# Performance work log

Hardware: AMD Instinct MI355X
Metric: run time of the kernel (lower is better)

## Reference

```python
import jax, jax.numpy as jnp
import numpy as np

DIM = 512
NUM_HEADS = 16
HEAD_DIM = DIM // NUM_HEADS  # 32
SCALE = HEAD_DIM ** -0.5
B_, N = 1024, 49  # num_windows*batch, window_size**2


def setup_inputs() -> dict:
    key = jax.random.key(0)
    ks = jax.random.split(key, 12)
    s = DIM ** -0.5
    return {
        "x": jax.random.normal(ks[0], (B_, N, DIM), jnp.float32),
        "x2": jax.random.normal(ks[1], (B_, N, DIM), jnp.float32),
        "x3": jax.random.normal(ks[2], (B_, N, DIM), jnp.float32),
        # Linear weights stored as [in, out] (y = x @ W + b), same math as torch Linear
        "Wqkv": jax.random.normal(ks[3], (DIM, 3 * DIM), jnp.float32) * s,
        "bqkv": jnp.zeros((3 * DIM,), jnp.float32),
        "Wqkv2": jax.random.normal(ks[4], (DIM, 3 * DIM), jnp.float32) * s,
        "bqkv2": jnp.zeros((3 * DIM,), jnp.float32),
        "Wgw": jax.random.normal(ks[5], (DIM, DIM), jnp.float32) * s,
        "bgw": jnp.zeros((DIM,), jnp.float32),
        "Wproj": jax.random.normal(ks[6], (DIM, DIM), jnp.float32) * s,
        "bproj": jnp.zeros((DIM,), jnp.float32),
        "a": jnp.zeros((1,), jnp.float32),
    }


def reference(x, x2, x3, Wqkv, bqkv, Wqkv2, bqkv2, Wgw, bgw, Wproj, bproj, a):
    B, Nn, C = x.shape
    H, D = NUM_HEADS, HEAD_DIM
    # qkv from x: only k is actually used downstream
    qkv = (x @ Wqkv + bqkv).reshape(B, Nn, 3, H, D)
    k = jnp.transpose(qkv[:, :, 1], (0, 2, 1, 3))  # [B,H,N,D]
    # qkv2 from x3: q1 (gated query) and v1 (value + residual)
    qkv1 = (x3 @ Wqkv2 + bqkv2).reshape(B, Nn, 3, H, D)
    q1 = jnp.transpose(qkv1[:, :, 0], (0, 2, 1, 3))  # [B,H,N,D]
    v1 = jnp.transpose(qkv1[:, :, 2], (0, 2, 1, 3))  # [B,H,N,D]
    # gate from x2
    gw = jnp.transpose((x2 @ Wgw + bgw).reshape(B, Nn, H, D), (0, 2, 1, 3))
    q = q1 * SCALE * gw
    attn = jax.nn.softmax(jnp.einsum("bhnd,bhmd->bhnm", q, k), axis=-1)
    out = jnp.einsum("bhnm,bhmd->bhnd", attn, v1) + v1 * a
    out = jnp.transpose(out, (0, 2, 1, 3)).reshape(B, Nn, C)
    return out @ Wproj + bproj
```

## Files before the change

### kernel.cpp

```cpp
#include <hip/hip_runtime.h>

#define MR 50176
#define DIMC 512
#define NWIN 49
#define NBATCH 1024
#define NHEADS 16
#define ATTN_SCALE 0.17677669529663689f

typedef short bf16x8 __attribute__((ext_vector_type(8)));
typedef float f32x4 __attribute__((ext_vector_type(4)));
typedef unsigned int u32;

__device__ __forceinline__ unsigned short f2bf(float f) {
  union { float f; u32 u; } v; v.f = f;
  u32 u = v.u;
  u += 0x7FFFu + ((u >> 16) & 1u);
  return (unsigned short)(u >> 16);
}
__device__ __forceinline__ float bits_f(u32 u) {
  union { u32 u; float f; } v; v.u = u; return v.f;
}

__device__ __forceinline__ size_t pk_chunk(int r, int c) {
  return (((size_t)(r >> 3) * 8 + (c >> 3)) * 64 +
          ((r & 7) * 8 + ((c & 7) ^ (r & 7)))) << 4;
}

typedef const __attribute__((address_space(1))) u32* gp_t;
typedef __attribute__((address_space(3))) u32* lp_t;
__device__ __forceinline__ void glds16(const void* g, void* l) {
  __builtin_amdgcn_global_load_lds((gp_t)g, (lp_t)l, 16, 0, 0);
}

__global__ __launch_bounds__(256) void prep_w_pack(
    const float* __restrict__ Wqkv, const float* __restrict__ Wqkv2,
    const float* __restrict__ Wgw, const float* __restrict__ Wproj,
    short* __restrict__ Wp) {
  const int tid = blockIdx.x * 256 + threadIdx.x;
  const int li = tid & 63, gl = tid >> 6;
  const int kline = gl & 7, group = gl >> 3;
  const int rr = li >> 3, pp = li & 7;
  const int row = group * 8 + rr;
  const int k = kline * 64 + ((pp ^ rr) << 3);
  const int n = row & 511, mat = row >> 9;
  const float* W; int ldw, col;
  if (mat == 0)      { W = Wqkv;  ldw = 1536; col = 512 + n; }
  else if (mat == 1) { W = Wqkv2; ldw = 1536; col = n; }
  else if (mat == 2) { W = Wqkv2; ldw = 1536; col = 1024 + n; }
  else if (mat == 3) { W = Wgw;   ldw = 512;  col = n; }
  else               { W = Wproj; ldw = 512;  col = n; }
  unsigned short h[8];
#pragma unroll
  for (int j = 0; j < 8; ++j) h[j] = f2bf(W[(size_t)(k + j) * ldw + col]);
  u32 w0 = (u32)h[0] | ((u32)h[1] << 16);
  u32 w1 = (u32)h[2] | ((u32)h[3] << 16);
  u32 w2 = (u32)h[4] | ((u32)h[5] << 16);
  u32 w3 = (u32)h[6] | ((u32)h[7] << 16);
  ((uint4*)Wp)[tid] = make_uint4(w0, w1, w2, w3);
}

struct GemmCfg {
  const short* A[4];
  const float* Af[4];
  const float* bias[4];
  short* out[4];
  int wrow0[4];
};

template <int LNX, bool OUT_F32, bool CONVA>
__global__ __launch_bounds__(256) void gemm_glds(
    GemmCfg cfg, const short* __restrict__ Wp, float* __restrict__ outf) {
  __shared__ short As[128 * 64];
  __shared__ short Bs[128 * 64];

  const int t = threadIdx.x, w = t >> 6, lane = t & 63;
  const int l15 = lane & 15, q = lane >> 4;
  const int wm = w >> 1, wn = w & 1;
  const int id = blockIdx.x;
  const int xcd = id & 7, slot = id >> 3;
  const int bx = slot & ((1 << LNX) - 1);
  const int y = xcd + ((slot >> LNX) << 3);
  const int row0 = y * 128;
  const int unit = bx >> 2, sub = bx & 3;
  const float* bias = cfg.bias[unit];
  short* outb = cfg.out[unit];
  const int nw0 = cfg.wrow0[unit] + sub * 128;
  const int col0 = sub * 128;

  f32x4 acc[4][4];
#pragma unroll
  for (int i = 0; i < 4; ++i)
#pragma unroll
    for (int j = 0; j < 4; ++j) acc[i][j] = {0.f, 0.f, 0.f, 0.f};

  const size_t lb = (size_t)lane * 16;
  const int r7 = l15 & 7, hi8 = l15 >> 3;

  if constexpr (CONVA) {
    const int rr = lane >> 3, pp = lane & 7;
    const float* abase =
        cfg.Af[unit] + (size_t)(row0 + w * 32 + rr) * DIMC + ((pp ^ rr) << 3);
    float4 ar[4][2];
#pragma unroll
    for (int jj = 0; jj < 4; ++jj) {
      const float* s = abase + (size_t)jj * 8 * DIMC;
      ar[jj][0] = *(const float4*)s;
      ar[jj][1] = *(const float4*)(s + 4);
    }
    for (int kt = 0; kt < 8; ++kt) {
      asm volatile("s_barrier" ::: "memory");
#pragma unroll
      for (int jj = 0; jj < 4; ++jj) {
        const int rg = w * 4 + jj;
        const char* gb =
            (const char*)Wp + ((((size_t)(nw0 >> 3) + rg) * 8 + kt) << 10);
        glds16(gb + lb, &Bs[(size_t)rg << 9]);
      }
      asm volatile("s_waitcnt vmcnt(4)" ::: "memory");
#pragma unroll
      for (int jj = 0; jj < 4; ++jj) {
        u32 w0 = (u32)f2bf(ar[jj][0].x) | ((u32)f2bf(ar[jj][0].y) << 16);
        u32 w1 = (u32)f2bf(ar[jj][0].z) | ((u32)f2bf(ar[jj][0].w) << 16);
        u32 w2 = (u32)f2bf(ar[jj][1].x) | ((u32)f2bf(ar[jj][1].y) << 16);
        u32 w3 = (u32)f2bf(ar[jj][1].z) | ((u32)f2bf(ar[jj][1].w) << 16);
        *(uint4*)&As[(((size_t)(w * 4 + jj)) << 9) + (size_t)lane * 8] =
            make_uint4(w0, w1, w2, w3);
      }
      if (kt < 7) {
#pragma unroll
        for (int jj = 0; jj < 4; ++jj) {
          const float* s = abase + (size_t)jj * 8 * DIMC + (kt + 1) * 64;
          ar[jj][0] = *(const float4*)s;
          ar[jj][1] = *(const float4*)(s + 4);
        }
        asm volatile("s_waitcnt vmcnt(8) lgkmcnt(0)" ::: "memory");
      } else {
        asm volatile("s_waitcnt vmcnt(0) lgkmcnt(0)" ::: "memory");
      }
      asm volatile("s_barrier" ::: "memory");
#pragma unroll
      for (int s = 0; s < 2; ++s) {
        const int sw = ((s * 4 + q) ^ r7);
        const int pos = (r7 * 8 + sw) * 8;
        bf16x8 af[4], bfr[4];
#pragma unroll
        for (int i = 0; i < 4; ++i)
          af[i] = *(const bf16x8*)&As[((wm * 8 + i * 2 + hi8) << 9) + pos];
#pragma unroll
        for (int j = 0; j < 4; ++j)
          bfr[j] = *(const bf16x8*)&Bs[((wn * 8 + j * 2 + hi8) << 9) + pos];
#pragma unroll
        for (int i = 0; i < 4; ++i)
#pragma unroll
          for (int j = 0; j < 4; ++j)
            acc[i][j] = __builtin_amdgcn_mfma_f32_16x16x32_bf16(
                af[i], bfr[j], acc[i][j], 0, 0, 0);
      }
    }
  } else {
    const short* Ap = cfg.A[unit];
    for (int kt = 0; kt < 8; ++kt) {
      __syncthreads();
#pragma unroll
      for (int jj = 0; jj < 4; ++jj) {
        const int rg = w * 4 + jj;
        const char* ga =
            (const char*)Ap + ((((size_t)(row0 >> 3) + rg) * 8 + kt) << 10);
        glds16(ga + lb, &As[(size_t)rg << 9]);
        const char* gb =
            (const char*)Wp + ((((size_t)(nw0 >> 3) + rg) * 8 + kt) << 10);
        glds16(gb + lb, &Bs[(size_t)rg << 9]);
      }
      __syncthreads();
#pragma unroll
      for (int s = 0; s < 2; ++s) {
        const int sw = ((s * 4 + q) ^ r7);
        const int pos = (r7 * 8 + sw) * 8;
        bf16x8 af[4], bfr[4];
#pragma unroll
        for (int i = 0; i < 4; ++i)
          af[i] = *(const bf16x8*)&As[((wm * 8 + i * 2 + hi8) << 9) + pos];
#pragma unroll
        for (int j = 0; j < 4; ++j)
          bfr[j] = *(const bf16x8*)&Bs[((wn * 8 + j * 2 + hi8) << 9) + pos];
#pragma unroll
        for (int i = 0; i < 4; ++i)
#pragma unroll
          for (int j = 0; j < 4; ++j)
            acc[i][j] = __builtin_amdgcn_mfma_f32_16x16x32_bf16(
                af[i], bfr[j], acc[i][j], 0, 0, 0);
      }
    }
  }

#pragma unroll
  for (int j = 0; j < 4; ++j) {
    const int C = col0 + wn * 64 + j * 16 + l15;
    const float bv = bias[C];
#pragma unroll
    for (int i = 0; i < 4; ++i) {
#pragma unroll
      for (int r = 0; r < 4; ++r) {
        const int R = row0 + wm * 64 + i * 16 + q * 4 + r;
        const float val = acc[i][j][r] + bv;
        if constexpr (OUT_F32)
          outf[(size_t)R * DIMC + C] = val;
        else
          *(short*)((char*)outb + pk_chunk(R, C >> 3) + ((C & 7) << 1)) =
              (short)f2bf(val);
      }
    }
  }
}

__global__ __launch_bounds__(256) void attn_mfma(
    const short* __restrict__ kbuf, const short* __restrict__ qbuf,
    const short* __restrict__ vbuf, const short* __restrict__ gbuf,
    const float* __restrict__ a_scalar, short* __restrict__ obuf) {
  __shared__ short pls[4][64 * 40];
  __shared__ short vls[4][32 * 72];

  const int t = threadIdx.x;
  const int w = t >> 6, lane = t & 63;
  const int l15 = lane & 15, q = lane >> 4;
  const int wid = blockIdx.x * 4 + w;
  const int b = wid >> 4, h = wid & 15;
  const int row0 = b * NWIN;
  const float aval = a_scalar[0];
  short* P = pls[w];
  short* VT = vls[w];

#pragma unroll
  for (int it = 0; it < 5; ++it) {
    int off = (it * 64 + lane) * 8;
    if (off < 32 * 72) *(uint4*)&VT[off] = make_uint4(0u, 0u, 0u, 0u);
  }

  bf16x8 kf[4];
#pragma unroll
  for (int mj = 0; mj < 4; ++mj) {
    int m = mj * 16 + l15; if (m > 48) m = 48;
    kf[mj] = *(const bf16x8*)((const char*)kbuf + pk_chunk(row0 + m, h * 4 + q));
  }
  bf16x8 qf[4];
#pragma unroll
  for (int mi = 0; mi < 4; ++mi) {
    int n = mi * 16 + l15; if (n > 48) n = 48;
    const size_t off = pk_chunk(row0 + n, h * 4 + q);
    uint4 qa = *(const uint4*)((const char*)qbuf + off);
    uint4 ga = *(const uint4*)((const char*)gbuf + off);
    u32* qa_ = (u32*)&qa;
    u32* ga_ = (u32*)&ga;
    uint4 res; u32* r_ = (u32*)&res;
#pragma unroll
    for (int jj = 0; jj < 4; ++jj) {
      float lo = bits_f(qa_[jj] << 16) * bits_f(ga_[jj] << 16);
      float hi = bits_f(qa_[jj] & 0xffff0000u) * bits_f(ga_[jj] & 0xffff0000u);
      r_[jj] = (u32)f2bf(lo) | ((u32)f2bf(hi) << 16);
    }
    qf[mi] = *(bf16x8*)&res;
  }
#pragma unroll
  for (int it = 0; it < 4; ++it) {
    int chunk = it * 64 + lane;
    if (chunk < 196) {
      int n = chunk >> 2, dcq = chunk & 3;
      uint4 v = *(const uint4*)((const char*)vbuf + pk_chunk(row0 + n, h * 4 + dcq));
      const short* vs = (const short*)&v;
#pragma unroll
      for (int j = 0; j < 8; ++j) VT[(dcq * 8 + j) * 72 + n] = vs[j];
    }
  }

  f32x4 s[4][4];
#pragma unroll
  for (int mi = 0; mi < 4; ++mi)
#pragma unroll
    for (int nj = 0; nj < 4; ++nj) {
      f32x4 z = {0.f, 0.f, 0.f, 0.f};
      s[mi][nj] = __builtin_amdgcn_mfma_f32_16x16x32_bf16(qf[mi], kf[nj], z, 0, 0, 0);
    }

#pragma unroll
  for (int mi = 0; mi < 4; ++mi)
#pragma unroll
    for (int nj = 0; nj < 4; ++nj) {
      const bool valid = (nj * 16 + l15) < NWIN;
#pragma unroll
      for (int r = 0; r < 4; ++r)
        s[mi][nj][r] = valid ? __expf(ATTN_SCALE * s[mi][nj][r]) : 0.f;
    }

  float lsum[4][4];
#pragma unroll
  for (int mi = 0; mi < 4; ++mi)
#pragma unroll
    for (int r = 0; r < 4; ++r) {
      float part = s[mi][0][r] + s[mi][1][r] + s[mi][2][r] + s[mi][3][r];
      part += __shfl_xor(part, 1, 64);
      part += __shfl_xor(part, 2, 64);
      part += __shfl_xor(part, 4, 64);
      part += __shfl_xor(part, 8, 64);
      lsum[mi][r] = part;
    }

  f32x4 o[4][2];
#pragma unroll
  for (int mi = 0; mi < 4; ++mi)
#pragma unroll
    for (int dj = 0; dj < 2; ++dj) o[mi][dj] = {0.f, 0.f, 0.f, 0.f};

#pragma unroll
  for (int c = 0; c < 2; ++c) {
#pragma unroll
    for (int mi = 0; mi < 4; ++mi)
#pragma unroll
      for (int njh = 0; njh < 2; ++njh) {
        const int nj = c * 2 + njh;
        const int m = nj * 16 + l15;
#pragma unroll
        for (int r = 0; r < 4; ++r) {
          const int n = mi * 16 + q * 4 + r;
          float val = s[mi][nj][r];
          if (m == n) val += aval * lsum[mi][r];
          P[n * 40 + njh * 16 + l15] = (short)f2bf(val);
        }
      }
    bf16x8 bfr[2];
#pragma unroll
    for (int dj = 0; dj < 2; ++dj)
      bfr[dj] = *(const bf16x8*)&VT[(dj * 16 + l15) * 72 + c * 32 + q * 8];
#pragma unroll
    for (int mi = 0; mi < 4; ++mi) {
      bf16x8 af = *(const bf16x8*)&P[(mi * 16 + l15) * 40 + q * 8];
#pragma unroll
      for (int dj = 0; dj < 2; ++dj)
        o[mi][dj] = __builtin_amdgcn_mfma_f32_16x16x32_bf16(af, bfr[dj],
                                                            o[mi][dj], 0, 0, 0);
    }
  }

#pragma unroll
  for (int mi = 0; mi < 4; ++mi)
#pragma unroll
    for (int r = 0; r < 4; ++r) {
      const int n = mi * 16 + q * 4 + r;
      if (n < NWIN) {
        const float rl = 1.0f / lsum[mi][r];
#pragma unroll
        for (int dj = 0; dj < 2; ++dj) {
          const int d = dj * 16 + l15;
          *(short*)((char*)obuf + pk_chunk(row0 + n, h * 4 + (d >> 3)) +
                    ((d & 7) << 1)) = (short)f2bf(o[mi][dj][r] * rl);
        }
      }
    }
}

extern "C" void kernel_launch(void* const* d_in, const int* in_sizes, int n_in,
                              void* d_out, int out_size, void* d_ws,
                              size_t ws_size, hipStream_t stream) {
  const float* x     = (const float*)d_in[0];
  const float* x2    = (const float*)d_in[1];
  const float* x3    = (const float*)d_in[2];
  const float* Wqkv  = (const float*)d_in[3];
  const float* bqkv  = (const float*)d_in[4];
  const float* Wqkv2 = (const float*)d_in[5];
  const float* bqkv2 = (const float*)d_in[6];
  const float* Wgw   = (const float*)d_in[7];
  const float* bgw   = (const float*)d_in[8];
  const float* Wproj = (const float*)d_in[9];
  const float* bproj = (const float*)d_in[10];
  const float* a     = (const float*)d_in[11];

  char* ws = (char*)d_ws;
  const size_t WTSZ = (size_t)2560 * DIMC * sizeof(short);
  const size_t BSZ  = (size_t)MR * DIMC * sizeof(short);
  short* wt_all = (short*)ws;

  short* kbuf = (short*)(ws + WTSZ);
  short* qbuf = (short*)(ws + WTSZ + BSZ);
  short* vbuf = (short*)(ws + WTSZ + 2 * BSZ);
  short* gbuf = (short*)(ws + WTSZ + 3 * BSZ);
  short* obuf = (short*)(ws + WTSZ + 4 * BSZ);

  prep_w_pack<<<640, 256, 0, stream>>>(Wqkv, Wqkv2, Wgw, Wproj, wt_all);

  GemmCfg s1 = {};
  s1.Af[0] = x;  s1.Af[1] = x3; s1.Af[2] = x3; s1.Af[3] = x2;
  s1.bias[0] = bqkv + 512; s1.bias[1] = bqkv2;
  s1.bias[2] = bqkv2 + 1024; s1.bias[3] = bgw;
  s1.out[0] = kbuf; s1.out[1] = qbuf; s1.out[2] = vbuf; s1.out[3] = gbuf;
  s1.wrow0[0] = 0; s1.wrow0[1] = 512; s1.wrow0[2] = 1024; s1.wrow0[3] = 1536;
  gemm_glds<4, false, true><<<16 * 392, 256, 0, stream>>>(s1, wt_all, nullptr);

  attn_mfma<<<(NBATCH * NHEADS) / 4, 256, 0, stream>>>(kbuf, qbuf, vbuf,
                                                       gbuf, a, obuf);

  GemmCfg pj = {};
  pj.A[0] = obuf; pj.bias[0] = bproj; pj.out[0] = nullptr; pj.wrow0[0] = 2048;
  gemm_glds<2, true, false><<<4 * 392, 256, 0, stream>>>(pj, wt_all,
                                                         (float*)d_out);
}
```

Measured before the change: 612.7 us.

## Double-buffer LDS tiles in GEMM to overlap loads with MFMA compute

Doubles the A and B shared-memory tiles so the next K-slice is staged, via global_load_lds and register-prefetched fp32 A conversion, while the current slice is multiplied. This drops one barrier per K-step and hides global load latency behind MFMA work. It uses inline-asm dwordx4 loads with manual vmcnt counting, which is fragile if the compiler reorders loads. LDS use rises to 64KB per block, which may lower occupancy.

```diff
diff --git a/kernel.cpp b/kernel.cpp
--- a/kernel.cpp
+++ b/kernel.cpp
@@ -30,6 +30,12 @@
 typedef __attribute__((address_space(3))) u32* lp_t;
 __device__ __forceinline__ void glds16(const void* g, void* l) {
   __builtin_amdgcn_global_load_lds((gp_t)g, (lp_t)l, 16, 0, 0);
+}
+
+__device__ __forceinline__ f32x4 gload4(const float* p) {
+  f32x4 r;
+  asm volatile("global_load_dwordx4 %0, %1, off" : "=v"(r) : "v"(p));
+  return r;
 }
 
 __global__ __launch_bounds__(256) void prep_w_pack(
@@ -70,8 +76,8 @@
 template <int LNX, bool OUT_F32, bool CONVA>
 __global__ __launch_bounds__(256) void gemm_glds(
     GemmCfg cfg, const short* __restrict__ Wp, float* __restrict__ outf) {
-  __shared__ short As[128 * 64];
-  __shared__ short Bs[128 * 64];
+  __shared__ short As[2][8192];
+  __shared__ short Bs[2][8192];
 
   const int t = threadIdx.x, w = t >> 6, lane = t & 63;
   const int l15 = lane & 15, q = lane >> 4;
@@ -96,102 +102,119 @@
   const size_t lb = (size_t)lane * 16;
   const int r7 = l15 & 7, hi8 = l15 >> 3;
 
+#define COMPUTE_TILE(SL)                                                      \
+  do {                                                                        \
+    _Pragma("unroll")                                                         \
+    for (int sk = 0; sk < 2; ++sk) {                                          \
+      const int sw = ((sk * 4 + q) ^ r7);                                     \
+      const int pos = (r7 * 8 + sw) * 8;                                      \
+      bf16x8 af[4], bfr[4];                                                   \
+      _Pragma("unroll")                                                       \
+      for (int i = 0; i < 4; ++i)                                             \
+        af[i] = *(const bf16x8*)&As[SL][((wm * 8 + i * 2 + hi8) << 9) + pos]; \
+      _Pragma("unroll")                                                       \
+      for (int j = 0; j < 4; ++j)                                             \
+        bfr[j] = *(const bf16x8*)&Bs[SL][((wn * 8 + j * 2 + hi8) << 9) + pos];\
+      _Pragma("unroll")                                                       \
+      for (int i = 0; i < 4; ++i)                                             \
+        _Pragma("unroll")                                                     \
+        for (int j = 0; j < 4; ++j)                                           \
+          acc[i][j] = __builtin_amdgcn_mfma_f32_16x16x32_bf16(                \
+              af[i], bfr[j], acc[i][j], 0, 0, 0);                             \
+    }                                                                         \
+  } while (0)
+
   if constexpr (CONVA) {
     const int rr = lane >> 3, pp = lane & 7;
     const float* abase =
         cfg.Af[unit] + (size_t)(row0 + w * 32 + rr) * DIMC + ((pp ^ rr) << 3);
-    float4 ar[4][2];
-#pragma unroll
-    for (int jj = 0; jj < 4; ++jj) {
-      const float* s = abase + (size_t)jj * 8 * DIMC;
-      ar[jj][0] = *(const float4*)s;
-      ar[jj][1] = *(const float4*)(s + 4);
-    }
-    for (int kt = 0; kt < 8; ++kt) {
-      asm volatile("s_barrier" ::: "memory");
+    f32x4 ar[4][2];
+
+    auto loadA = [&](int kt2) {
+#pragma unroll
+      for (int jj = 0; jj < 4; ++jj) {
+        const float* s = abase + (size_t)jj * 8 * DIMC + kt2 * 64;
+        ar[jj][0] = gload4(s);
+        ar[jj][1] = gload4(s + 4);
+      }
+    };
+    auto stageB = [&](int kt2) {
+      const int sl = kt2 & 1;
 #pragma unroll
       for (int jj = 0; jj < 4; ++jj) {
         const int rg = w * 4 + jj;
         const char* gb =
-            (const char*)Wp + ((((size_t)(nw0 >> 3) + rg) * 8 + kt) << 10);
-        glds16(gb + lb, &Bs[(size_t)rg << 9]);
-      }
-      asm volatile("s_waitcnt vmcnt(4)" ::: "memory");
+            (const char*)Wp + ((((size_t)(nw0 >> 3) + rg) * 8 + kt2) << 10);
+        glds16(gb + lb, &Bs[sl][(size_t)rg << 9]);
+      }
+    };
+    auto packA = [&](int sl) {
 #pragma unroll
       for (int jj = 0; jj < 4; ++jj) {
-        u32 w0 = (u32)f2bf(ar[jj][0].x) | ((u32)f2bf(ar[jj][0].y) << 16);
-        u32 w1 = (u32)f2bf(ar[jj][0].z) | ((u32)f2bf(ar[jj][0].w) << 16);
-        u32 w2 = (u32)f2bf(ar[jj][1].x) | ((u32)f2bf(ar[jj][1].y) << 16);
-        u32 w3 = (u32)f2bf(ar[jj][1].z) | ((u32)f2bf(ar[jj][1].w) << 16);
-        *(uint4*)&As[(((size_t)(w * 4 + jj)) << 9) + (size_t)lane * 8] =
+        u32 w0 = (u32)f2bf(ar[jj][0][0]) | ((u32)f2bf(ar[jj][0][1]) << 16);
+        u32 w1 = (u32)f2bf(ar[jj][0][2]) | ((u32)f2bf(ar[jj][0][3]) << 16);
+        u32 w2 = (u32)f2bf(ar[jj][1][0]) | ((u32)f2bf(ar[jj][1][1]) << 16);
+        u32 w3 = (u32)f2bf(ar[jj][1][2]) | ((u32)f2bf(ar[jj][1][3]) << 16);
+        *(uint4*)&As[sl][(((size_t)(w * 4 + jj)) << 9) + (size_t)lane * 8] =
             make_uint4(w0, w1, w2, w3);
       }
+    };
+
+    loadA(0);
+    __builtin_amdgcn_sched_barrier(0);
+    stageB(0);
+    asm volatile("s_waitcnt vmcnt(4)" ::: "memory");
+    __builtin_amdgcn_sched_barrier(0);
+    packA(0);
+    loadA(1);
+    asm volatile("s_waitcnt vmcnt(8) lgkmcnt(0)" ::: "memory");
+    asm volatile("s_barrier" ::: "memory");
+
+    for (int kt = 0; kt < 8; ++kt) {
+      const int s = kt & 1;
       if (kt < 7) {
-#pragma unroll
-        for (int jj = 0; jj < 4; ++jj) {
-          const float* s = abase + (size_t)jj * 8 * DIMC + (kt + 1) * 64;
-          ar[jj][0] = *(const float4*)s;
-          ar[jj][1] = *(const float4*)(s + 4);
-        }
+        stageB(kt + 1);
+        asm volatile("s_waitcnt vmcnt(4)" ::: "memory");
+        __builtin_amdgcn_sched_barrier(0);
+        packA(s ^ 1);
+        if (kt < 6) loadA(kt + 2);
+      }
+      COMPUTE_TILE(s);
+      if (kt < 6)
         asm volatile("s_waitcnt vmcnt(8) lgkmcnt(0)" ::: "memory");
-      } else {
+      else if (kt == 6)
         asm volatile("s_waitcnt vmcnt(0) lgkmcnt(0)" ::: "memory");
-      }
-      asm volatile("s_barrier" ::: "memory");
-#pragma unroll
-      for (int s = 0; s < 2; ++s) {
-        const int sw = ((s * 4 + q) ^ r7);
-        const int pos = (r7 * 8 + sw) * 8;
-        bf16x8 af[4], bfr[4];
-#pragma unroll
-        for (int i = 0; i < 4; ++i)
-          af[i] = *(const bf16x8*)&As[((wm * 8 + i * 2 + hi8) << 9) + pos];
-#pragma unroll
-        for (int j = 0; j < 4; ++j)
-          bfr[j] = *(const bf16x8*)&Bs[((wn * 8 + j * 2 + hi8) << 9) + pos];
-#pragma unroll
-        for (int i = 0; i < 4; ++i)
-#pragma unroll
-          for (int j = 0; j < 4; ++j)
-            acc[i][j] = __builtin_amdgcn_mfma_f32_16x16x32_bf16(
-                af[i], bfr[j], acc[i][j], 0, 0, 0);
-      }
+      if (kt < 7) asm volatile("s_barrier" ::: "memory");
     }
   } else {
     const short* Ap = cfg.A[unit];
-    for (int kt = 0; kt < 8; ++kt) {
-      __syncthreads();
+    auto stageAB = [&](int kt2) {
+      const int sl = kt2 & 1;
 #pragma unroll
       for (int jj = 0; jj < 4; ++jj) {
         const int rg = w * 4 + jj;
         const char* ga =
-            (const char*)Ap + ((((size_t)(row0 >> 3) + rg) * 8 + kt) << 10);
-        glds16(ga + lb, &As[(size_t)rg << 9]);
+            (const char*)Ap + ((((size_t)(row0 >> 3) + rg) * 8 + kt2) << 10);
+        glds16(ga + lb, &As[sl][(size_t)rg << 9]);
         const char* gb =
-            (const char*)Wp + ((((size_t)(nw0 >> 3) + rg) * 8 + kt) << 10);
-        glds16(gb + lb, &Bs[(size_t)rg << 9]);
-      }
-      __syncthreads();
-#pragma unroll
-      for (int s = 0; s < 2; ++s) {
-        const int sw = ((s * 4 + q) ^ r7);
-        const int pos = (r7 * 8 + sw) * 8;
-        bf16x8 af[4], bfr[4];
-#pragma unroll
-        for (int i = 0; i < 4; ++i)
-          af[i] = *(const bf16x8*)&As[((wm * 8 + i * 2 + hi8) << 9) + pos];
-#pragma unroll
-        for (int j = 0; j < 4; ++j)
-          bfr[j] = *(const bf16x8*)&Bs[((wn * 8 + j * 2 + hi8) << 9) + pos];
-#pragma unroll
-        for (int i = 0; i < 4; ++i)
-#pragma unroll
-          for (int j = 0; j < 4; ++j)
-            acc[i][j] = __builtin_amdgcn_mfma_f32_16x16x32_bf16(
-                af[i], bfr[j], acc[i][j], 0, 0, 0);
-      }
-    }
-  }
+            (const char*)Wp + ((((size_t)(nw0 >> 3) + rg) * 8 + kt2) << 10);
+        glds16(gb + lb, &Bs[sl][(size_t)rg << 9]);
+      }
+    };
+    stageAB(0);
+    asm volatile("s_waitcnt vmcnt(0)" ::: "memory");
+    asm volatile("s_barrier" ::: "memory");
+    for (int kt = 0; kt < 8; ++kt) {
+      const int s = kt & 1;
+      if (kt < 7) stageAB(kt + 1);
+      COMPUTE_TILE(s);
+      if (kt < 7) {
+        asm volatile("s_waitcnt vmcnt(0) lgkmcnt(0)" ::: "memory");
+        asm volatile("s_barrier" ::: "memory");
+      }
+    }
+  }
+#undef COMPUTE_TILE
 
 #pragma unroll
   for (int j = 0; j < 4; ++j) {
```

Result: faster. 556.9 us (-9.1%).
